# Kernel optimization log

Hardware: AMD Instinct MI355X
Metric: run time of the kernel (lower is better)

The kernel has to match this reference:

```python
import jax, jax.numpy as jnp
import numpy as np

V, E, U, B, T = 32000, 256, 512, 64, 256  # vocab, embed_dim, enc_units, batch, seq_len


def setup_inputs() -> dict:
    key = jax.random.key(0)
    ks = jax.random.split(key, 8)
    x = jax.random.randint(ks[0], (B, T), 0, V)  # int ids; 0 = mask token
    emb = jax.random.normal(ks[1], (V, E), dtype=jnp.float32) * 0.02
    W_f = jax.random.normal(ks[2], (E, 4 * U), dtype=jnp.float32) * 0.05
    R_f = jax.random.normal(ks[3], (U, 4 * U), dtype=jnp.float32) * 0.05
    b_f = jnp.zeros((4 * U,), dtype=jnp.float32)
    W_b = jax.random.normal(ks[4], (E, 4 * U), dtype=jnp.float32) * 0.05
    R_b = jax.random.normal(ks[5], (U, 4 * U), dtype=jnp.float32) * 0.05
    b_b = jnp.zeros((4 * U,), dtype=jnp.float32)
    return {"x": x, "emb": emb, "W_f": W_f, "R_f": R_f, "b_f": b_f,
            "W_b": W_b, "R_b": R_b, "b_b": b_b}


def _lstm_scan(e_seq, m_seq, W, R, b):
    # e_seq: [T,B,E], m_seq: [T,B,1] bool. Keras LSTM with recurrent_activation='tanh':
    # i,f,o gates use tanh (non-default!), candidate and cell-output use tanh.
    x_proj = jnp.einsum('tbe,eg->tbg', e_seq, W) + b  # precompute input projection [T,B,4U]
    h0 = jnp.zeros((e_seq.shape[1], U), dtype=e_seq.dtype)
    c0 = jnp.zeros_like(h0)

    def step(carry, inp):
        h, c = carry
        xz, m = inp
        z = xz + h @ R  # [B,4U]
        zi, zf, zg, zo = jnp.split(z, 4, axis=-1)
        i = jnp.tanh(zi)
        f = jnp.tanh(zf)
        g = jnp.tanh(zg)
        o = jnp.tanh(zo)
        c_new = f * c + i * g
        h_new = o * jnp.tanh(c_new)
        # Keras masking: masked steps carry previous state/output through
        h = jnp.where(m, h_new, h)
        c = jnp.where(m, c_new, c)
        return (h, c), h

    (hT, cT), hs = jax.lax.scan(step, (h0, c0), (x_proj, m_seq))
    return hs, hT  # [T,B,U], [B,U]


def reference(x, emb, W_f, R_f, b_f, W_b, R_b, b_b):
    mask = (x != 0)  # mask_zero=True
    e = emb[x]                      # [B,T,E] embedding lookup
    e_t = jnp.swapaxes(e, 0, 1)     # [T,B,E]
    m_t = jnp.swapaxes(mask, 0, 1)[:, :, None]  # [T,B,1]
    # forward direction
    h_fwd, _ = _lstm_scan(e_t, m_t, W_f, R_f, b_f)
    # backward direction: reverse time, scan, reverse outputs back (Keras Bidirectional)
    h_bwd_rev, backward_h = _lstm_scan(e_t[::-1], m_t[::-1], W_b, R_b, b_b)
    h_bwd = h_bwd_rev[::-1]
    final_output = jnp.swapaxes(jnp.concatenate([h_fwd, h_bwd], axis=-1), 0, 1)  # [B,T,2U]
    return final_output, backward_h
```

## Files before the change

kernel.cpp:

```cpp
#include <hip/hip_runtime.h>

#define V_ 32000
#define E_ 256
#define U_ 512
#define B_ 64
#define T_ 256
#define G_ 2048

#define RSTR 516
#define ASTR 260
#define WESTR 132


#define GLDS16(gsrc, ldst) __builtin_amdgcn_global_load_lds( \
    (const __attribute__((address_space(1))) void*)(gsrc),    \
    (__attribute__((address_space(3))) void*)(ldst), 16, 0, 0)

__global__ __launch_bounds__(512, 1)
void bilstm_kernel(const int* __restrict__ x,
                   const float* __restrict__ emb,
                   const float* __restrict__ Wf, const float* __restrict__ Rf,
                   const float* __restrict__ bf,
                   const float* __restrict__ Wb, const float* __restrict__ Rb,
                   const float* __restrict__ bb,
                   float* __restrict__ out, float* __restrict__ hbuf,
                   unsigned* __restrict__ bar, float* __restrict__ xz,
                   int CH)
{
    __shared__ __align__(16) float Rl[32 * RSTR];
    __shared__ __align__(16) float HA[64 * ASTR];
    __shared__ __align__(16) float Wel[32 * WESTR];

    const int blk = blockIdx.x;
    const int dir = blk >> 7;
    const int rem = blk & 127;
    const int u0 = (rem >> 1) * 8;
    const int b0base = (rem & 1) * 32;
    const int grp = dir * 2 + (rem & 1);
    const int mem = rem >> 1;
    unsigned* myslot = bar + (grp * 64 + mem) * 16;

    const int tid   = threadIdx.x;
    const int wv    = tid >> 6;
    const int lane  = tid & 63;
    const int uu    = lane & 7;
    const int blgrp = lane >> 3;
    const int blf   = tid >> 3;
    const int fuu   = tid & 7;

    const float* Wd = dir ? Wb : Wf;
    const float* Rd = dir ? Rb : Rf;
    const float* bd = dir ? bb : bf;

    {
        const int sgc  = tid & 31;
        const int gcol = ((sgc >> 3) * 512) + u0 + (sgc & 7);
        for (int k = tid >> 5; k < 512; k += 16)
            Rl[sgc * RSTR + k] = Rd[(size_t)k * G_ + gcol];
    }
    float bias4[4];
    #pragma unroll
    for (int g = 0; g < 4; ++g) bias4[g] = bd[g * 512 + u0 + fuu];

    float c_reg = 0.0f;
    float h_prev = 0.0f;
    const float4* Rl4  = reinterpret_cast<const float4*>(Rl);
    const float4* HA4  = reinterpret_cast<const float4*>(HA);
    const float4* Wel4 = reinterpret_cast<const float4*>(Wel);
    float4* HAw4 = reinterpret_cast<float4*>(HA);
    float4* P4s = reinterpret_cast<float4*>(Wel);
    float4* P4p = reinterpret_cast<float4*>(HA);

    __syncthreads();

    const int nch = T_ / CH;
    for (int ch = 0; ch < nch; ++ch) {
        const int nat = CH >> 1;
        for (int at = 0; at < nat; ++at) {
            __syncthreads();
            for (int i = 0; i < 8; ++i) {
                int rr   = wv * 8 + i;
                int tloc = at * 2 + (rr >> 5);
                int bla  = rr & 31;
                int sg   = ch * CH + tloc;
                int tea  = dir ? (T_ - 1 - sg) : sg;
                int tok  = x[(b0base + bla) * T_ + tea];
                GLDS16(emb + (size_t)tok * E_ + lane * 4, HA + rr * ASTR);
            }
            float pacc[8][4];
            #pragma unroll
            for (int j = 0; j < 8; ++j)
                #pragma unroll
                for (int g = 0; g < 4; ++g) pacc[j][g] = 0.0f;

            for (int kh = 0; kh < 2; ++kh) {
                if (kh) __syncthreads();
                {
                    const int sgc  = tid & 31;
                    const int gcol = ((sgc >> 3) * 512) + u0 + (sgc & 7);
                    for (int kk = tid >> 5; kk < 128; kk += 16)
                        Wel[sgc * WESTR + kk] = Wd[(size_t)(kh * 128 + kk) * G_ + gcol];
                }
                __syncthreads();
                #pragma unroll
                for (int k4 = 0; k4 < 4; ++k4) {
                    const int kw = wv * 4 + k4;
                    float4 w0 = Wel4[(0 * 8 + uu) * 33 + kw];
                    float4 w1 = Wel4[(1 * 8 + uu) * 33 + kw];
                    float4 w2 = Wel4[(2 * 8 + uu) * 33 + kw];
                    float4 w3 = Wel4[(3 * 8 + uu) * 33 + kw];
                    #pragma unroll
                    for (int j = 0; j < 8; ++j) {
                        float4 a = HA4[(blgrp + 8 * j) * 65 + kh * 32 + kw];
                        pacc[j][0] = fmaf(w0.x,a.x,pacc[j][0]); pacc[j][0] = fmaf(w0.y,a.y,pacc[j][0]);
                        pacc[j][0] = fmaf(w0.z,a.z,pacc[j][0]); pacc[j][0] = fmaf(w0.w,a.w,pacc[j][0]);
                        pacc[j][1] = fmaf(w1.x,a.x,pacc[j][1]); pacc[j][1] = fmaf(w1.y,a.y,pacc[j][1]);
                        pacc[j][1] = fmaf(w1.z,a.z,pacc[j][1]); pacc[j][1] = fmaf(w1.w,a.w,pacc[j][1]);
                        pacc[j][2] = fmaf(w2.x,a.x,pacc[j][2]); pacc[j][2] = fmaf(w2.y,a.y,pacc[j][2]);
                        pacc[j][2] = fmaf(w2.z,a.z,pacc[j][2]); pacc[j][2] = fmaf(w2.w,a.w,pacc[j][2]);
                        pacc[j][3] = fmaf(w3.x,a.x,pacc[j][3]); pacc[j][3] = fmaf(w3.y,a.y,pacc[j][3]);
                        pacc[j][3] = fmaf(w3.z,a.z,pacc[j][3]); pacc[j][3] = fmaf(w3.w,a.w,pacc[j][3]);
                    }
                }
            }
            __syncthreads();
            #pragma unroll
            for (int j = 0; j < 8; ++j)
                P4p[(wv * 64 + blgrp + 8 * j) * 8 + uu] =
                    float4{pacc[j][0], pacc[j][1], pacc[j][2], pacc[j][3]};
            __syncthreads();
            {
                const int r   = tid >> 3;
                const int uq  = tid & 7;
                const int tl  = at * 2 + (r >> 5);
                const int bla = r & 31;
                float* dst = xz + ((size_t)blk * CH + tl) * 1024;
                float4 s = P4p[(0 * 64 + r) * 8 + uq];
                #pragma unroll
                for (int q = 1; q < 8; ++q) {
                    float4 p = P4p[(q * 64 + r) * 8 + uq];
                    s.x += p.x; s.y += p.y; s.z += p.z; s.w += p.w;
                }
                dst[(0 * 8 + uq) * 32 + bla] = s.x;
                dst[(1 * 8 + uq) * 32 + bla] = s.y;
                dst[(2 * 8 + uq) * 32 + bla] = s.z;
                dst[(3 * 8 + uq) * 32 + bla] = s.w;
            }
        }
        __syncthreads();

        for (int sc = 0; sc < CH; ++sc) {
            const int s   = ch * CH + sc;
            const int te  = dir ? (T_ - 1 - s) : s;
            const int cur = s & 1, nxt = cur ^ 1;

            int mtok = 0;
            float xzv[4] = {0.f, 0.f, 0.f, 0.f};
            if (tid < 256) {
                mtok = x[(b0base + blf) * T_ + te];
                const float* xzp = xz + ((size_t)blk * CH + sc) * 1024;
                #pragma unroll
                for (int g = 0; g < 4; ++g)
                    xzv[g] = xzp[(g * 8 + fuu) * 32 + blf] + bias4[g];
            }

            if (s > 0) {
                unsigned* slot = bar + (grp * 64 + wv * 8 + (lane & 7)) * 16;
                while (__hip_atomic_load(slot, __ATOMIC_RELAXED,
                                         __HIP_MEMORY_SCOPE_AGENT) < (unsigned)s)
                    __builtin_amdgcn_s_sleep(1);
            }

            {
                const float* hsrc = hbuf + ((size_t)(cur * 2 + dir) * B_ + b0base) * U_;
                const int cl = lane & 15;
                const int rl = lane >> 4;
                #pragma unroll
                for (int i = 0; i < 8; ++i) {
                    const int row = rl + 4 * i;
                    const unsigned long long* p = (const unsigned long long*)
                        (hsrc + (size_t)row * U_ + wv * 64 + cl * 4);
                    unsigned long long a = __hip_atomic_load(p,     __ATOMIC_RELAXED,
                                                             __HIP_MEMORY_SCOPE_AGENT);
                    unsigned long long b = __hip_atomic_load(p + 1, __ATOMIC_RELAXED,
                                                             __HIP_MEMORY_SCOPE_AGENT);
                    float2 fa = __builtin_bit_cast(float2, a);
                    float2 fb = __builtin_bit_cast(float2, b);
                    HAw4[row * 129 + wv * 16 + cl] = float4{fa.x, fa.y, fb.x, fb.y};
                }
            }

            float pz[4][4];
            #pragma unroll
            for (int j = 0; j < 4; ++j)
                #pragma unroll
                for (int g = 0; g < 4; ++g) pz[j][g] = 0.0f;
            const int kbase = wv * 16;
            #pragma unroll 4
            for (int k4 = 0; k4 < 16; ++k4) {
                const int kk = kbase + k4;
                float4 h0 = HA4[(blgrp + 8 * 0) * 129 + kk];
                float4 h1 = HA4[(blgrp + 8 * 1) * 129 + kk];
                float4 h2 = HA4[(blgrp + 8 * 2) * 129 + kk];
                float4 h3 = HA4[(blgrp + 8 * 3) * 129 + kk];
                #pragma unroll
                for (int g = 0; g < 4; ++g) {
                    float4 w = Rl4[(g * 8 + uu) * 129 + kk];
                    pz[0][g] = fmaf(w.x,h0.x,pz[0][g]); pz[0][g] = fmaf(w.y,h0.y,pz[0][g]);
                    pz[0][g] = fmaf(w.z,h0.z,pz[0][g]); pz[0][g] = fmaf(w.w,h0.w,pz[0][g]);
                    pz[1][g] = fmaf(w.x,h1.x,pz[1][g]); pz[1][g] = fmaf(w.y,h1.y,pz[1][g]);
                    pz[1][g] = fmaf(w.z,h1.z,pz[1][g]); pz[1][g] = fmaf(w.w,h1.w,pz[1][g]);
                    pz[2][g] = fmaf(w.x,h2.x,pz[2][g]); pz[2][g] = fmaf(w.y,h2.y,pz[2][g]);
                    pz[2][g] = fmaf(w.z,h2.z,pz[2][g]); pz[2][g] = fmaf(w.w,h2.w,pz[2][g]);
                    pz[3][g] = fmaf(w.x,h3.x,pz[3][g]); pz[3][g] = fmaf(w.y,h3.y,pz[3][g]);
                    pz[3][g] = fmaf(w.z,h3.z,pz[3][g]); pz[3][g] = fmaf(w.w,h3.w,pz[3][g]);
                }
            }

            if (wv >= 4) {
                #pragma unroll
                for (int j = 0; j < 4; ++j)
                    P4s[((wv - 4) * 32 + blgrp + 8 * j) * 8 + uu] =
                        float4{pz[j][0], pz[j][1], pz[j][2], pz[j][3]};
            }
            __syncthreads();
            if (wv < 4) {
                #pragma unroll
                for (int j = 0; j < 4; ++j) {
                    const int idx = (wv * 32 + blgrp + 8 * j) * 8 + uu;
                    float4 t = P4s[idx];
                    t.x += pz[j][0]; t.y += pz[j][1];
                    t.z += pz[j][2]; t.w += pz[j][3];
                    P4s[idx] = t;
                }
            }
            __syncthreads();

            if (tid < 256) {
                float4 z0 = P4s[(0 * 32 + blf) * 8 + fuu];
                float4 z1 = P4s[(1 * 32 + blf) * 8 + fuu];
                float4 z2 = P4s[(2 * 32 + blf) * 8 + fuu];
                float4 z3 = P4s[(3 * 32 + blf) * 8 + fuu];
                float fi = tanhf(z0.x + z1.x + z2.x + z3.x + xzv[0]);
                float ff = tanhf(z0.y + z1.y + z2.y + z3.y + xzv[1]);
                float fg = tanhf(z0.z + z1.z + z2.z + z3.z + xzv[2]);
                float fo = tanhf(z0.w + z1.w + z2.w + z3.w + xzv[3]);
                float cn = fmaf(ff, c_reg, fi * fg);
                float hn = fo * tanhf(cn);
                bool  m  = (mtok != 0);
                float hsel = m ? hn : h_prev;
                c_reg = m ? cn : c_reg;
                h_prev = hsel;

                const int b = b0base + blf;
                __hip_atomic_store(&hbuf[((size_t)(nxt * 2 + dir) * B_ + b) * U_ + u0 + fuu],
                                   hsel, __ATOMIC_RELAXED, __HIP_MEMORY_SCOPE_AGENT);
                out[((size_t)b * T_ + te) * 1024 + dir * 512 + u0 + fuu] = hsel;
                if (dir == 1 && s == T_ - 1)
                    out[(size_t)B_ * T_ * 1024 + (size_t)b * U_ + u0 + fuu] = hsel;
            }

            __syncthreads();
            if (tid == 0)
                __hip_atomic_store(myslot, (unsigned)(s + 1), __ATOMIC_RELAXED,
                                   __HIP_MEMORY_SCOPE_AGENT);
        }
    }
}

extern "C" void kernel_launch(void* const* d_in, const int* in_sizes, int n_in,
                              void* d_out, int out_size, void* d_ws, size_t ws_size,
                              hipStream_t stream) {
    const int*   x   = (const int*)d_in[0];
    const float* emb = (const float*)d_in[1];
    const float* Wf  = (const float*)d_in[2];
    const float* Rf  = (const float*)d_in[3];
    const float* bfp = (const float*)d_in[4];
    const float* Wb  = (const float*)d_in[5];
    const float* Rb  = (const float*)d_in[6];
    const float* bbp = (const float*)d_in[7];
    float* out  = (float*)d_out;
    float* hbuf = (float*)d_ws;
    unsigned* bar = (unsigned*)((char*)d_ws + 512 * 1024);
    float* xzbuf  = (float*)((char*)d_ws + (1 << 20));

    int CH = 32;
    while (CH > 2 && (size_t)(CH + 1) * (1 << 20) > ws_size) CH >>= 1;

    hipMemsetAsync(hbuf, 0, (size_t)2 * B_ * U_ * sizeof(float), stream);
    hipMemsetAsync(bar, 0, 4 * 64 * 16 * sizeof(unsigned), stream);

    void* args[] = {
        (void*)&x, (void*)&emb,
        (void*)&Wf, (void*)&Rf, (void*)&bfp,
        (void*)&Wb, (void*)&Rb, (void*)&bbp,
        (void*)&out, (void*)&hbuf, (void*)&bar, (void*)&xzbuf, (void*)&CH
    };
    hipLaunchCooperativeKernel((const void*)bilstm_kernel,
                               dim3(256), dim3(512), args, 0, stream);
}
```

Measured before the change: 3.443 ms.

## Double block size to 1024 threads and reduce recurrent partials with LDS atomics

Launches 1024 threads per block and splits the recurrent h@R K-dimension across 16 waves instead of 8, so each wave does half the FMAs per timestep. The two-stage LDS partial-sum reduction is replaced by LDS atomicAdd into a zeroed padded buffer, which the gate threads read and reset. The input-projection phase stays on the first 512 threads while the rest idle. Risks: more register pressure under the 1024-thread launch bound, LDS atomic contention, and the float summation order now varies between runs.

```diff
diff --git a/kernel.cpp b/kernel.cpp
--- a/kernel.cpp
+++ b/kernel.cpp
@@ -10,13 +10,14 @@
 #define RSTR 516
 #define ASTR 260
 #define WESTR 132
+#define PSTR 36
 
 
 #define GLDS16(gsrc, ldst) __builtin_amdgcn_global_load_lds( \
     (const __attribute__((address_space(1))) void*)(gsrc),    \
     (__attribute__((address_space(3))) void*)(ldst), 16, 0, 0)
 
-__global__ __launch_bounds__(512, 1)
+__global__ __launch_bounds__(1024, 1)
 void bilstm_kernel(const int* __restrict__ x,
                    const float* __restrict__ emb,
                    const float* __restrict__ Wf, const float* __restrict__ Rf,
@@ -55,7 +56,7 @@
     {
         const int sgc  = tid & 31;
         const int gcol = ((sgc >> 3) * 512) + u0 + (sgc & 7);
-        for (int k = tid >> 5; k < 512; k += 16)
+        for (int k = tid >> 5; k < 512; k += 32)
             Rl[sgc * RSTR + k] = Rd[(size_t)k * G_ + gcol];
     }
     float bias4[4];
@@ -68,7 +69,7 @@
     const float4* HA4  = reinterpret_cast<const float4*>(HA);
     const float4* Wel4 = reinterpret_cast<const float4*>(Wel);
     float4* HAw4 = reinterpret_cast<float4*>(HA);
-    float4* P4s = reinterpret_cast<float4*>(Wel);
+    float*  Psum = Wel;
     float4* P4p = reinterpret_cast<float4*>(HA);
 
     __syncthreads();
@@ -78,14 +79,16 @@
         const int nat = CH >> 1;
         for (int at = 0; at < nat; ++at) {
             __syncthreads();
-            for (int i = 0; i < 8; ++i) {
-                int rr   = wv * 8 + i;
-                int tloc = at * 2 + (rr >> 5);
-                int bla  = rr & 31;
-                int sg   = ch * CH + tloc;
-                int tea  = dir ? (T_ - 1 - sg) : sg;
-                int tok  = x[(b0base + bla) * T_ + tea];
-                GLDS16(emb + (size_t)tok * E_ + lane * 4, HA + rr * ASTR);
+            if (tid < 512) {
+                for (int i = 0; i < 8; ++i) {
+                    int rr   = wv * 8 + i;
+                    int tloc = at * 2 + (rr >> 5);
+                    int bla  = rr & 31;
+                    int sg   = ch * CH + tloc;
+                    int tea  = dir ? (T_ - 1 - sg) : sg;
+                    int tok  = x[(b0base + bla) * T_ + tea];
+                    GLDS16(emb + (size_t)tok * E_ + lane * 4, HA + rr * ASTR);
+                }
             }
             float pacc[8][4];
             #pragma unroll
@@ -95,41 +98,45 @@
 
             for (int kh = 0; kh < 2; ++kh) {
                 if (kh) __syncthreads();
-                {
+                if (tid < 512) {
                     const int sgc  = tid & 31;
                     const int gcol = ((sgc >> 3) * 512) + u0 + (sgc & 7);
                     for (int kk = tid >> 5; kk < 128; kk += 16)
                         Wel[sgc * WESTR + kk] = Wd[(size_t)(kh * 128 + kk) * G_ + gcol];
                 }
                 __syncthreads();
-                #pragma unroll
-                for (int k4 = 0; k4 < 4; ++k4) {
-                    const int kw = wv * 4 + k4;
-                    float4 w0 = Wel4[(0 * 8 + uu) * 33 + kw];
-                    float4 w1 = Wel4[(1 * 8 + uu) * 33 + kw];
-                    float4 w2 = Wel4[(2 * 8 + uu) * 33 + kw];
-                    float4 w3 = Wel4[(3 * 8 + uu) * 33 + kw];
+                if (tid < 512) {
                     #pragma unroll
-                    for (int j = 0; j < 8; ++j) {
-                        float4 a = HA4[(blgrp + 8 * j) * 65 + kh * 32 + kw];
-                        pacc[j][0] = fmaf(w0.x,a.x,pacc[j][0]); pacc[j][0] = fmaf(w0.y,a.y,pacc[j][0]);
-                        pacc[j][0] = fmaf(w0.z,a.z,pacc[j][0]); pacc[j][0] = fmaf(w0.w,a.w,pacc[j][0]);
-                        pacc[j][1] = fmaf(w1.x,a.x,pacc[j][1]); pacc[j][1] = fmaf(w1.y,a.y,pacc[j][1]);
-                        pacc[j][1] = fmaf(w1.z,a.z,pacc[j][1]); pacc[j][1] = fmaf(w1.w,a.w,pacc[j][1]);
-                        pacc[j][2] = fmaf(w2.x,a.x,pacc[j][2]); pacc[j][2] = fmaf(w2.y,a.y,pacc[j][2]);
-                        pacc[j][2] = fmaf(w2.z,a.z,pacc[j][2]); pacc[j][2] = fmaf(w2.w,a.w,pacc[j][2]);
-                        pacc[j][3] = fmaf(w3.x,a.x,pacc[j][3]); pacc[j][3] = fmaf(w3.y,a.y,pacc[j][3]);
-                        pacc[j][3] = fmaf(w3.z,a.z,pacc[j][3]); pacc[j][3] = fmaf(w3.w,a.w,pacc[j][3]);
+                    for (int k4 = 0; k4 < 4; ++k4) {
+                        const int kw = wv * 4 + k4;
+                        float4 w0 = Wel4[(0 * 8 + uu) * 33 + kw];
+                        float4 w1 = Wel4[(1 * 8 + uu) * 33 + kw];
+                        float4 w2 = Wel4[(2 * 8 + uu) * 33 + kw];
+                        float4 w3 = Wel4[(3 * 8 + uu) * 33 + kw];
+                        #pragma unroll
+                        for (int j = 0; j < 8; ++j) {
+                            float4 a = HA4[(blgrp + 8 * j) * 65 + kh * 32 + kw];
+                            pacc[j][0] = fmaf(w0.x,a.x,pacc[j][0]); pacc[j][0] = fmaf(w0.y,a.y,pacc[j][0]);
+                            pacc[j][0] = fmaf(w0.z,a.z,pacc[j][0]); pacc[j][0] = fmaf(w0.w,a.w,pacc[j][0]);
+                            pacc[j][1] = fmaf(w1.x,a.x,pacc[j][1]); pacc[j][1] = fmaf(w1.y,a.y,pacc[j][1]);
+                            pacc[j][1] = fmaf(w1.z,a.z,pacc[j][1]); pacc[j][1] = fmaf(w1.w,a.w,pacc[j][1]);
+                            pacc[j][2] = fmaf(w2.x,a.x,pacc[j][2]); pacc[j][2] = fmaf(w2.y,a.y,pacc[j][2]);
+                            pacc[j][2] = fmaf(w2.z,a.z,pacc[j][2]); pacc[j][2] = fmaf(w2.w,a.w,pacc[j][2]);
+                            pacc[j][3] = fmaf(w3.x,a.x,pacc[j][3]); pacc[j][3] = fmaf(w3.y,a.y,pacc[j][3]);
+                            pacc[j][3] = fmaf(w3.z,a.z,pacc[j][3]); pacc[j][3] = fmaf(w3.w,a.w,pacc[j][3]);
+                        }
                     }
                 }
             }
             __syncthreads();
-            #pragma unroll
-            for (int j = 0; j < 8; ++j)
-                P4p[(wv * 64 + blgrp + 8 * j) * 8 + uu] =
-                    float4{pacc[j][0], pacc[j][1], pacc[j][2], pacc[j][3]};
-            __syncthreads();
-            {
+            if (tid < 512) {
+                #pragma unroll
+                for (int j = 0; j < 8; ++j)
+                    P4p[(wv * 64 + blgrp + 8 * j) * 8 + uu] =
+                        float4{pacc[j][0], pacc[j][1], pacc[j][2], pacc[j][3]};
+            }
+            __syncthreads();
+            if (tid < 512) {
                 const int r   = tid >> 3;
                 const int uq  = tid & 7;
                 const int tl  = at * 2 + (r >> 5);
@@ -147,6 +154,7 @@
                 dst[(3 * 8 + uq) * 32 + bla] = s.w;
             }
         }
+        if (tid < 576) { Psum[tid] = 0.0f; Psum[tid + 576] = 0.0f; }
         __syncthreads();
 
         for (int sc = 0; sc < CH; ++sc) {
@@ -165,7 +173,7 @@
             }
 
             if (s > 0) {
-                unsigned* slot = bar + (grp * 64 + wv * 8 + (lane & 7)) * 16;
+                unsigned* slot = bar + (grp * 64 + wv * 4 + (lane & 3)) * 16;
                 while (__hip_atomic_load(slot, __ATOMIC_RELAXED,
                                          __HIP_MEMORY_SCOPE_AGENT) < (unsigned)s)
                     __builtin_amdgcn_s_sleep(1);
@@ -173,20 +181,20 @@
 
             {
                 const float* hsrc = hbuf + ((size_t)(cur * 2 + dir) * B_ + b0base) * U_;
-                const int cl = lane & 15;
-                const int rl = lane >> 4;
-                #pragma unroll
-                for (int i = 0; i < 8; ++i) {
-                    const int row = rl + 4 * i;
+                const int cl = lane & 7;
+                const int rl = lane >> 3;
+                #pragma unroll
+                for (int i = 0; i < 4; ++i) {
+                    const int row = rl + 8 * i;
                     const unsigned long long* p = (const unsigned long long*)
-                        (hsrc + (size_t)row * U_ + wv * 64 + cl * 4);
+                        (hsrc + (size_t)row * U_ + (wv * 8 + cl) * 4);
                     unsigned long long a = __hip_atomic_load(p,     __ATOMIC_RELAXED,
                                                              __HIP_MEMORY_SCOPE_AGENT);
                     unsigned long long b = __hip_atomic_load(p + 1, __ATOMIC_RELAXED,
                                                              __HIP_MEMORY_SCOPE_AGENT);
                     float2 fa = __builtin_bit_cast(float2, a);
                     float2 fb = __builtin_bit_cast(float2, b);
-                    HAw4[row * 129 + wv * 16 + cl] = float4{fa.x, fa.y, fb.x, fb.y};
+                    HAw4[row * 129 + wv * 8 + cl] = float4{fa.x, fa.y, fb.x, fb.y};
                 }
             }
 
@@ -195,9 +203,9 @@
             for (int j = 0; j < 4; ++j)
                 #pragma unroll
                 for (int g = 0; g < 4; ++g) pz[j][g] = 0.0f;
-            const int kbase = wv * 16;
-            #pragma unroll 4
-            for (int k4 = 0; k4 < 16; ++k4) {
+            const int kbase = wv * 8;
+            #pragma unroll
+            for (int k4 = 0; k4 < 8; ++k4) {
                 const int kk = kbase + k4;
                 float4 h0 = HA4[(blgrp + 8 * 0) * 129 + kk];
                 float4 h1 = HA4[(blgrp + 8 * 1) * 129 + kk];
@@ -217,34 +225,24 @@
                 }
             }
 
-            if (wv >= 4) {
-                #pragma unroll
-                for (int j = 0; j < 4; ++j)
-                    P4s[((wv - 4) * 32 + blgrp + 8 * j) * 8 + uu] =
-                        float4{pz[j][0], pz[j][1], pz[j][2], pz[j][3]};
-            }
-            __syncthreads();
-            if (wv < 4) {
-                #pragma unroll
-                for (int j = 0; j < 4; ++j) {
-                    const int idx = (wv * 32 + blgrp + 8 * j) * 8 + uu;
-                    float4 t = P4s[idx];
-                    t.x += pz[j][0]; t.y += pz[j][1];
-                    t.z += pz[j][2]; t.w += pz[j][3];
-                    P4s[idx] = t;
-                }
-            }
+            #pragma unroll
+            for (int j = 0; j < 4; ++j)
+                #pragma unroll
+                for (int g = 0; g < 4; ++g)
+                    atomicAdd(&Psum[(blgrp + 8 * j) * PSTR + g * 8 + uu], pz[j][g]);
+
             __syncthreads();
 
             if (tid < 256) {
-                float4 z0 = P4s[(0 * 32 + blf) * 8 + fuu];
-                float4 z1 = P4s[(1 * 32 + blf) * 8 + fuu];
-                float4 z2 = P4s[(2 * 32 + blf) * 8 + fuu];
-                float4 z3 = P4s[(3 * 32 + blf) * 8 + fuu];
-                float fi = tanhf(z0.x + z1.x + z2.x + z3.x + xzv[0]);
-                float ff = tanhf(z0.y + z1.y + z2.y + z3.y + xzv[1]);
-                float fg = tanhf(z0.z + z1.z + z2.z + z3.z + xzv[2]);
-                float fo = tanhf(z0.w + z1.w + z2.w + z3.w + xzv[3]);
+                const int pbase = blf * PSTR + fuu;
+                float zi = Psum[pbase + 0];  Psum[pbase + 0]  = 0.0f;
+                float zf = Psum[pbase + 8];  Psum[pbase + 8]  = 0.0f;
+                float zg = Psum[pbase + 16]; Psum[pbase + 16] = 0.0f;
+                float zo = Psum[pbase + 24]; Psum[pbase + 24] = 0.0f;
+                float fi = tanhf(zi + xzv[0]);
+                float ff = tanhf(zf + xzv[1]);
+                float fg = tanhf(zg + xzv[2]);
+                float fo = tanhf(zo + xzv[3]);
                 float cn = fmaf(ff, c_reg, fi * fg);
                 float hn = fo * tanhf(cn);
                 bool  m  = (mtok != 0);
@@ -297,5 +295,5 @@
         (void*)&out, (void*)&hbuf, (void*)&bar, (void*)&xzbuf, (void*)&CH
     };
     hipLaunchCooperativeKernel((const void*)bilstm_kernel,
-                               dim3(256), dim3(512), args, 0, stream);
+                               dim3(256), dim3(1024), args, 0, stream);
 }
```

New measurement: 8.691 ms. +152.5%, slower.
